# Kernel optimization log

Measured on AMD Instinct MI355X. Metric: run time of the kernel, lower is better.

## Reference

```python
import jax, jax.numpy as jnp
import numpy as np

N_HEAD = 12

def setup_inputs() -> dict:
    key = jax.random.key(0)
    ks = jax.random.split(key, 5)
    B, T, C = 2, 2048, 768
    s = 1.0 / np.sqrt(C)
    return {
        "x": jax.random.normal(ks[0], (B, T, C), dtype=jnp.float32),
        "W_qkv": jax.random.normal(ks[1], (C, 3 * C), dtype=jnp.float32) * s,
        "b_qkv": jnp.zeros((3 * C,), dtype=jnp.float32),
        "W_proj": jax.random.normal(ks[2], (C, C), dtype=jnp.float32) * s,
        "b_proj": jnp.zeros((C,), dtype=jnp.float32),
    }

def reference(x, W_qkv, b_qkv, W_proj, b_proj):
    B, T, C = x.shape
    H = N_HEAD
    D = C // H
    qkv = x @ W_qkv + b_qkv                      # [B,T,3C]
    qkv = qkv.reshape(B, T, 3, H, D)
    q = jnp.transpose(qkv[:, :, 0], (0, 2, 1, 3))  # [B,H,T,D]
    k = jnp.transpose(qkv[:, :, 1], (0, 2, 1, 3))
    v = jnp.transpose(qkv[:, :, 2], (0, 2, 1, 3))
    scale = 1.0 / np.sqrt(D).astype(np.float32)
    att = jnp.einsum('bhqd,bhkd->bhqk', q, k) * scale  # [B,H,T,T]
    causal = jnp.tril(jnp.ones((T, T), dtype=bool))
    att = jnp.where(causal, att, -jnp.inf)
    att = jax.nn.softmax(att, axis=-1)
    out = jnp.einsum('bhqk,bhkd->bhqd', att, v)   # [B,H,T,D]
    out = jnp.transpose(out, (0, 2, 1, 3)).reshape(B, T, C)
    return out @ W_proj + b_proj
```

## Files before the change

kernel.cpp:

```cpp
#include <hip/hip_runtime.h>
#include <stdint.h>

typedef short short8 __attribute__((ext_vector_type(8)));
typedef short short4v __attribute__((ext_vector_type(4)));
typedef float f32x4 __attribute__((ext_vector_type(4)));
typedef unsigned int u32x2 __attribute__((ext_vector_type(2)));
typedef unsigned int u32x4 __attribute__((ext_vector_type(4)));
typedef unsigned short u16;
typedef unsigned int u32;

#define T_ 2048
#define QK_SCALE 0.180336878f

__device__ inline u16 f2bf(float f) {
  unsigned u = __builtin_bit_cast(unsigned, f);
  u += 0x7fffu + ((u >> 16) & 1u);
  return (u16)(u >> 16);
}

__device__ inline u32 cvt_pk_bf16(float lo, float hi) {
  u32 r;
  asm("v_cvt_pk_bf16_f32 %0, %1, %2" : "=v"(r) : "v"(lo), "v"(hi));
  return r;
}

__device__ inline f32x4 mfma_bf16(short8 a, short8 b, f32x4 c) {
  return __builtin_amdgcn_mfma_f32_16x16x32_bf16(a, b, c, 0, 0, 0);
}

__device__ inline void gload16(const u16* g, u16* l) {
  __builtin_amdgcn_global_load_lds(
      (const __attribute__((address_space(1))) void*)g,
      (__attribute__((address_space(3))) void*)l, 16, 0, 0);
}


__device__ inline void tile_transpose(const float* __restrict__ W, u16* __restrict__ Wt,
                                      int R, int Ccols, int c0, int r0, int t,
                                      float (*tile)[33]) {
  int tr = t >> 3, tc = (t & 7) * 4;
  float4 v = *(const float4*)&W[(size_t)(r0 + tr) * Ccols + c0 + tc];
  tile[tr][tc + 0] = v.x; tile[tr][tc + 1] = v.y;
  tile[tr][tc + 2] = v.z; tile[tr][tc + 3] = v.w;
  __syncthreads();
  short4v o;
#pragma unroll
  for (int i = 0; i < 4; ++i) o[i] = (short)f2bf(tile[tc + i][tr]);
  *(short4v*)&Wt[(size_t)(c0 + tr) * R + r0 + tc] = o;
}

__global__ __launch_bounds__(256) void prep_kernel(const float* __restrict__ x,
                                                   const float* __restrict__ Wqkv,
                                                   const float* __restrict__ Wproj,
                                                   u16* __restrict__ xb,
                                                   u16* __restrict__ wqkvT,
                                                   u16* __restrict__ wprojT) {
  __shared__ float tile[32][33];
  int bid = blockIdx.x, t = threadIdx.x;
  if (bid < 3072) {
    int i = (bid * 256 + t) * 4;
    float4 v = *(const float4*)&x[i];
    short4v o;
    o[0] = (short)f2bf(v.x); o[1] = (short)f2bf(v.y);
    o[2] = (short)f2bf(v.z); o[3] = (short)f2bf(v.w);
    *(short4v*)&xb[i] = o;
  } else if (bid < 3072 + 1728) {
    int t2 = bid - 3072;
    tile_transpose(Wqkv, wqkvT, 768, 2304, (t2 % 72) * 32, (t2 / 72) * 32, t, tile);
  } else {
    int t3 = bid - 4800;
    tile_transpose(Wproj, wprojT, 768, 768, (t3 % 24) * 32, (t3 / 24) * 32, t, tile);
  }
}


template <int MODE, int MTILE>
__global__ __launch_bounds__(256) void gemm_kernel(const u16* __restrict__ A,
                                                   const u16* __restrict__ Bt,
                                                   const float* __restrict__ bias,
                                                   u16* __restrict__ qb,
                                                   u16* __restrict__ kb,
                                                   u16* __restrict__ vpb,
                                                   float* __restrict__ out) {
  constexpr int MF = MTILE / 32;
  __shared__ u16 S[MTILE * 64 + 8192];
  u16* As = S;
  u16* Bs = S + MTILE * 64;
  int tid = threadIdx.x, w = tid >> 6, l = tid & 63, lg = l >> 4, lr = l & 15;
  int nwg = gridDim.x * gridDim.y;
  int hw = blockIdx.y * gridDim.x + blockIdx.x;
  int logical = (hw & 7) * (nwg >> 3) + (hw >> 3);
  int n0 = (logical % gridDim.x) * 128, m0 = (logical / gridDim.x) * MTILE;
  int wm = (w >> 1) * (MTILE / 2), wn = (w & 1) * 64;
  f32x4 acc[MF][4] = {};
  int rsub = l >> 3;
  int sc = ((l & 7) ^ rsub) * 8;
  for (int kt = 0; kt < 12; ++kt) {
    int k0 = kt * 64;
    __syncthreads();
#pragma unroll
    for (int j = 0; j < MF; ++j) {
      int row = w * (MTILE / 4) + j * 8 + rsub;
      gload16(&A[(size_t)(m0 + row) * 768 + k0 + sc], &As[(w * MF + j) * 512]);
    }
#pragma unroll
    for (int j = 0; j < 4; ++j) {
      int row = w * 32 + j * 8 + rsub;
      gload16(&Bt[(size_t)(n0 + row) * 768 + k0 + sc], &Bs[(w * 4 + j) * 512]);
    }
    __syncthreads();
    short8 a[MF][2], b[4][2];
#pragma unroll
    for (int h = 0; h < 2; ++h) {
#pragma unroll
      for (int mf = 0; mf < MF; ++mf) {
        int cw = ((h * 4 + lg) ^ (lr & 7)) * 8;
        a[mf][h] = *(const short8*)&As[(wm + mf * 16 + lr) * 64 + cw];
      }
#pragma unroll
      for (int nf = 0; nf < 4; ++nf) {
        int cw = ((h * 4 + lg) ^ (lr & 7)) * 8;
        b[nf][h] = *(const short8*)&Bs[(wn + nf * 16 + lr) * 64 + cw];
      }
    }
#pragma unroll
    for (int h = 0; h < 2; ++h)
#pragma unroll
      for (int mf = 0; mf < MF; ++mf)
#pragma unroll
        for (int nf = 0; nf < 4; ++nf)
          acc[mf][nf] = mfma_bf16(a[mf][h], b[nf][h], acc[mf][nf]);
  }

  if constexpr (MODE == 0) {
    int sec = (n0 >= 1536) ? 2 : (n0 >= 768 ? 1 : 0);
    int ncol0 = n0 - sec * 768;
    if (sec < 2) {
#pragma unroll
      for (int nf = 0; nf < 4; ++nf) {
        int nn = wn + nf * 16 + lr;
        float bv = bias[n0 + nn];
        int c = ncol0 + nn;
        int hh = c >> 6, d = c & 63;
#pragma unroll
        for (int mf = 0; mf < MF; ++mf)
#pragma unroll
          for (int rr = 0; rr < 4; ++rr) {
            int m = m0 + wm + mf * 16 + 4 * lg + rr;
            int bb = m >> 11, tt = m & 2047;
            int bh = bb * 12 + hh;
            float v = acc[mf][nf][rr] + bv;
            if (sec == 0) qb[((size_t)bh * T_ + tt) * 64 + d] = f2bf(v * QK_SCALE);
            else          kb[((size_t)bh * T_ + tt) * 64 + d] = f2bf(v);
          }
      }
    } else {
      __syncthreads();
#pragma unroll
      for (int nf = 0; nf < 4; ++nf) {
        int row = wn + nf * 16 + lr;
        float bv = bias[n0 + row];
        int swz = (row & 7) << 3;
#pragma unroll
        for (int mf = 0; mf < MF; ++mf) {
          int pcol0 = wm + (mf >> 1) * 32 + 8 * lg + 4 * (mf & 1);
          u32x2 pk;
          pk[0] = cvt_pk_bf16(acc[mf][nf][0] + bv, acc[mf][nf][1] + bv);
          pk[1] = cvt_pk_bf16(acc[mf][nf][2] + bv, acc[mf][nf][3] + bv);
          *(u32x2*)&S[row * MTILE + (pcol0 ^ swz)] = pk;
        }
      }
      __syncthreads();
      constexpr int CPT = MTILE / 2;
      int rowo = tid >> 1, half = tid & 1;
      int c = ncol0 + rowo;
      int d = c & 63, hh = c >> 6;
      int bh = (m0 >> 11) * 12 + hh;
      u16* dst = vpb + ((size_t)bh * 64 + d) * T_ + (m0 & 2047) + half * CPT;
      int swzo = (rowo & 7) << 3;
#pragma unroll
      for (int i = 0; i < CPT / 8; ++i) {
        int col = half * CPT + i * 8;
        uint4 v = *(const uint4*)&S[rowo * MTILE + (col ^ swzo)];
        *(uint4*)&dst[i * 8] = v;
      }
    }
  } else {
#pragma unroll
    for (int nf = 0; nf < 4; ++nf) {
      int n = n0 + wn + nf * 16 + lr;
      float bv = bias[n];
#pragma unroll
      for (int mf = 0; mf < MF; ++mf)
#pragma unroll
        for (int rr = 0; rr < 4; ++rr) {
          int m = m0 + wm + mf * 16 + 4 * lg + rr;
          out[(size_t)m * 768 + n] = acc[mf][nf][rr] + bv;
        }
    }
  }
}


__global__ __launch_bounds__(256) void attn_kernel(const u16* __restrict__ Q,
                                                   const u16* __restrict__ K,
                                                   const u16* __restrict__ Vp,
                                                   u16* __restrict__ O) {
  __shared__ u16 sh[16384];
  int tid = threadIdx.x;
  int w = tid >> 6, l = tid & 63, lg = l >> 4, lr = l & 15;
  int idx = blockIdx.x;
  int head = idx % 24;
  int qblk = 31 - idx / 24;
  int b = head / 12, h = head % 12;
  int q0 = qblk * 64;
  int q0w = q0 + w * 16;
  const u16* Qb = Q + (size_t)head * T_ * 64;
  const u16* Kb = K + (size_t)head * T_ * 64;
  const u16* Vb = Vp + (size_t)head * 64 * T_;

  short8 qf0 = *(const short8*)&Qb[(size_t)(q0w + lr) * 64 + 8 * lg];
  short8 qf1 = *(const short8*)&Qb[(size_t)(q0w + lr) * 64 + 32 + 8 * lg];

  f32x4 ao[4] = {};
  float lrow = 0.f;
  int rsub = l >> 3;
  int scs = ((l & 7) ^ rsub) * 8;
  const int nt = qblk + 1;

#pragma unroll
  for (int j = 0; j < 2; ++j) {
    int ci = w * 2 + j;
    int row = ci * 8 + rsub;
    gload16(&Kb[(size_t)row * 64 + scs], &sh[ci * 512]);
    gload16(&Vb[(size_t)row * T_ + scs], &sh[8192 + ci * 512]);
  }
  __syncthreads();

  for (int t = 0; t < nt; ++t) {
    int cur = t & 1;
    int k0 = t * 64;
    if (t + 1 < nt) {
      int k1 = k0 + 64;
#pragma unroll
      for (int j = 0; j < 2; ++j) {
        int ci = w * 2 + j;
        int row = ci * 8 + rsub;
        gload16(&Kb[(size_t)(k1 + row) * 64 + scs], &sh[(cur ^ 1) * 4096 + ci * 512]);
        gload16(&Vb[(size_t)row * T_ + k1 + scs], &sh[8192 + (cur ^ 1) * 4096 + ci * 512]);
      }
    }
    if (k0 <= q0w + 15) {
      const u16* ks = sh + cur * 4096;
      const u16* vs = sh + 8192 + cur * 4096;
      f32x4 s[4];
      __builtin_amdgcn_s_setprio(1);
#pragma unroll
      for (int kg = 0; kg < 4; ++kg) {
        short8 ka0 = *(const short8*)&ks[(kg * 16 + lr) * 64 + ((lg ^ (lr & 7)) * 8)];
        short8 ka1 = *(const short8*)&ks[(kg * 16 + lr) * 64 + (((4 + lg) ^ (lr & 7)) * 8)];
        f32x4 z = {};
        z = mfma_bf16(ka0, qf0, z);
        z = mfma_bf16(ka1, qf1, z);
        s[kg] = z;
      }
      __builtin_amdgcn_s_setprio(0);
      int qa = q0w + lr;
      bool domask = (k0 + 63 > q0w);
      float sv[16];
      float ps = 0.f;
#pragma unroll
      for (int kg = 0; kg < 4; ++kg)
#pragma unroll
        for (int rr = 0; rr < 4; ++rr) {
          float x = s[kg][rr];
          if (domask) {
            int key = k0 + kg * 16 + 4 * lg + rr;
            x = (key <= qa) ? x : -1e30f;
          }
          float p = __builtin_amdgcn_exp2f(x);
          sv[kg * 4 + rr] = p;
          ps += p;
        }
      ps += __shfl_xor(ps, 16);
      ps += __shfl_xor(ps, 32);
      lrow += ps;
      short8 pb[2];
#pragma unroll
      for (int c = 0; c < 2; ++c) {
        u32x4 uu;
        uu[0] = cvt_pk_bf16(sv[c * 8 + 0], sv[c * 8 + 1]);
        uu[1] = cvt_pk_bf16(sv[c * 8 + 2], sv[c * 8 + 3]);
        uu[2] = cvt_pk_bf16(sv[c * 8 + 4], sv[c * 8 + 5]);
        uu[3] = cvt_pk_bf16(sv[c * 8 + 6], sv[c * 8 + 7]);
        pb[c] = __builtin_bit_cast(short8, uu);
      }
      __builtin_amdgcn_s_setprio(1);
#pragma unroll
      for (int dt = 0; dt < 4; ++dt) {
        short8 va0 = *(const short8*)&vs[(dt * 16 + lr) * 64 + ((lg ^ (lr & 7)) * 8)];
        short8 va1 = *(const short8*)&vs[(dt * 16 + lr) * 64 + (((4 + lg) ^ (lr & 7)) * 8)];
        ao[dt] = mfma_bf16(va0, pb[0], ao[dt]);
        ao[dt] = mfma_bf16(va1, pb[1], ao[dt]);
      }
      __builtin_amdgcn_s_setprio(0);
    }
    __syncthreads();
  }

  u16* ow = sh + w * 1152;
  float inv = 1.0f / lrow;
#pragma unroll
  for (int dt = 0; dt < 4; ++dt) {
    u32x2 pk;
    pk[0] = cvt_pk_bf16(ao[dt][0] * inv, ao[dt][1] * inv);
    pk[1] = cvt_pk_bf16(ao[dt][2] * inv, ao[dt][3] * inv);
    *(u32x2*)&ow[lr * 72 + dt * 16 + 4 * lg] = pk;
  }
  __syncthreads();
  int r = l >> 2, hc = l & 3;
  const u16* srow = sh + w * 1152 + r * 72 + hc * 16;
  u16* dst = O + ((size_t)(b * T_ + q0w + r)) * 768 + h * 64 + hc * 16;
  *(uint4*)&dst[0] = *(const uint4*)&srow[0];
  *(uint4*)&dst[8] = *(const uint4*)&srow[8];
}


extern "C" void kernel_launch(void* const* d_in, const int* in_sizes, int n_in,
                              void* d_out, int out_size, void* d_ws, size_t ws_size,
                              hipStream_t stream) {
  const float* x     = (const float*)d_in[0];
  const float* Wqkv  = (const float*)d_in[1];
  const float* bqkv  = (const float*)d_in[2];
  const float* Wproj = (const float*)d_in[3];
  const float* bproj = (const float*)d_in[4];
  float* out = (float*)d_out;
  char* ws = (char*)d_ws;
  u16* xb     = (u16*)(ws);
  u16* wqkvT  = (u16*)(ws + 6291456);
  u16* wprojT = (u16*)(ws + 9830400);
  u16* qb     = (u16*)(ws + 11010048);
  u16* kb     = (u16*)(ws + 17301504);
  u16* vpb    = (u16*)(ws + 23592960);
  u16* ob     = (u16*)(ws + 29884416);

  prep_kernel<<<5376, 256, 0, stream>>>(x, Wqkv, Wproj, xb, wqkvT, wprojT);
  gemm_kernel<0, 64><<<dim3(18, 64), 256, 0, stream>>>(xb, wqkvT, bqkv, qb, kb, vpb, nullptr);
  attn_kernel<<<768, 256, 0, stream>>>(qb, kb, vpb, ob);
  gemm_kernel<1, 64><<<dim3(6, 64), 256, 0, stream>>>(ob, wprojT, bproj, nullptr, nullptr, nullptr, out);
}
```

Measured before the change: 86.27 us.

## Split long causal attention query blocks across two workgroups with a combine pass

Query blocks 16–31, which carry the longest causal key ranges, are now split in half along the key dimension. Each half is computed by its own workgroup and writes unnormalised bf16 partial outputs and row sums into reused workspace buffers. A new combine kernel adds the two halves and normalises them. The aim is to balance load and raise the number of workgroups in flight. The cost is an extra kernel launch, more global traffic, and an extra bf16 rounding of the partial sums.

```diff
diff --git a/kernel.cpp b/kernel.cpp
--- a/kernel.cpp
+++ b/kernel.cpp
@@ -16,6 +16,10 @@
   unsigned u = __builtin_bit_cast(unsigned, f);
   u += 0x7fffu + ((u >> 16) & 1u);
   return (u16)(u >> 16);
+}
+
+__device__ inline float bf2f(u16 v) {
+  return __builtin_bit_cast(float, (u32)v << 16);
 }
 
 __device__ inline u32 cvt_pk_bf16(float lo, float hi) {
@@ -205,15 +209,21 @@
 __global__ __launch_bounds__(256) void attn_kernel(const u16* __restrict__ Q,
                                                    const u16* __restrict__ K,
                                                    const u16* __restrict__ Vp,
-                                                   u16* __restrict__ O) {
+                                                   u16* __restrict__ O,
+                                                   u16* __restrict__ Pp,
+                                                   float* __restrict__ Lp) {
   __shared__ u16 sh[16384];
   int tid = threadIdx.x;
   int w = tid >> 6, l = tid & 63, lg = l >> 4, lr = l & 15;
-  int idx = blockIdx.x;
-  int head = idx % 24;
-  int qblk = 31 - idx / 24;
+  int u = blockIdx.x;
+  int head = u % 24;
+  int v = u / 24;
+  int s, c;
+  if (v < 32) { s = 31 - (v >> 1); c = v & 1; }
+  else        { s = 47 - v; c = 0; }
+  bool ispartial = (v < 32);
   int b = head / 12, h = head % 12;
-  int q0 = qblk * 64;
+  int q0 = s * 64;
   int q0w = q0 + w * 16;
   const u16* Qb = Q + (size_t)head * T_ * 64;
   const u16* Kb = K + (size_t)head * T_ * 64;
@@ -226,21 +236,24 @@
   float lrow = 0.f;
   int rsub = l >> 3;
   int scs = ((l & 7) ^ rsub) * 8;
-  const int nt = qblk + 1;
+  int nt = s + 1;
+  int h1 = (s + 2) >> 1;
+  int t0 = (ispartial && c) ? h1 : 0;
+  int tEnd = (ispartial && !c) ? h1 : nt;
 
 #pragma unroll
   for (int j = 0; j < 2; ++j) {
     int ci = w * 2 + j;
     int row = ci * 8 + rsub;
-    gload16(&Kb[(size_t)row * 64 + scs], &sh[ci * 512]);
-    gload16(&Vb[(size_t)row * T_ + scs], &sh[8192 + ci * 512]);
+    gload16(&Kb[(size_t)(t0 * 64 + row) * 64 + scs], &sh[ci * 512]);
+    gload16(&Vb[(size_t)row * T_ + t0 * 64 + scs], &sh[8192 + ci * 512]);
   }
   __syncthreads();
 
-  for (int t = 0; t < nt; ++t) {
-    int cur = t & 1;
+  for (int t = t0; t < tEnd; ++t) {
+    int cur = (t - t0) & 1;
     int k0 = t * 64;
-    if (t + 1 < nt) {
+    if (t + 1 < tEnd) {
       int k1 = k0 + 64;
 #pragma unroll
       for (int j = 0; j < 2; ++j) {
@@ -253,7 +266,7 @@
     if (k0 <= q0w + 15) {
       const u16* ks = sh + cur * 4096;
       const u16* vs = sh + 8192 + cur * 4096;
-      f32x4 s[4];
+      f32x4 sm[4];
       __builtin_amdgcn_s_setprio(1);
 #pragma unroll
       for (int kg = 0; kg < 4; ++kg) {
@@ -262,7 +275,7 @@
         f32x4 z = {};
         z = mfma_bf16(ka0, qf0, z);
         z = mfma_bf16(ka1, qf1, z);
-        s[kg] = z;
+        sm[kg] = z;
       }
       __builtin_amdgcn_s_setprio(0);
       int qa = q0w + lr;
@@ -273,7 +286,7 @@
       for (int kg = 0; kg < 4; ++kg)
 #pragma unroll
         for (int rr = 0; rr < 4; ++rr) {
-          float x = s[kg][rr];
+          float x = sm[kg][rr];
           if (domask) {
             int key = k0 + kg * 16 + 4 * lg + rr;
             x = (key <= qa) ? x : -1e30f;
@@ -287,13 +300,13 @@
       lrow += ps;
       short8 pb[2];
 #pragma unroll
-      for (int c = 0; c < 2; ++c) {
+      for (int c2 = 0; c2 < 2; ++c2) {
         u32x4 uu;
-        uu[0] = cvt_pk_bf16(sv[c * 8 + 0], sv[c * 8 + 1]);
-        uu[1] = cvt_pk_bf16(sv[c * 8 + 2], sv[c * 8 + 3]);
-        uu[2] = cvt_pk_bf16(sv[c * 8 + 4], sv[c * 8 + 5]);
-        uu[3] = cvt_pk_bf16(sv[c * 8 + 6], sv[c * 8 + 7]);
-        pb[c] = __builtin_bit_cast(short8, uu);
+        uu[0] = cvt_pk_bf16(sv[c2 * 8 + 0], sv[c2 * 8 + 1]);
+        uu[1] = cvt_pk_bf16(sv[c2 * 8 + 2], sv[c2 * 8 + 3]);
+        uu[2] = cvt_pk_bf16(sv[c2 * 8 + 4], sv[c2 * 8 + 5]);
+        uu[3] = cvt_pk_bf16(sv[c2 * 8 + 6], sv[c2 * 8 + 7]);
+        pb[c2] = __builtin_bit_cast(short8, uu);
       }
       __builtin_amdgcn_s_setprio(1);
 #pragma unroll
@@ -309,7 +322,7 @@
   }
 
   u16* ow = sh + w * 1152;
-  float inv = 1.0f / lrow;
+  float inv = ispartial ? 1.0f : (1.0f / lrow);
 #pragma unroll
   for (int dt = 0; dt < 4; ++dt) {
     u32x2 pk;
@@ -320,9 +333,38 @@
   __syncthreads();
   int r = l >> 2, hc = l & 3;
   const u16* srow = sh + w * 1152 + r * 72 + hc * 16;
-  u16* dst = O + ((size_t)(b * T_ + q0w + r)) * 768 + h * 64 + hc * 16;
-  *(uint4*)&dst[0] = *(const uint4*)&srow[0];
-  *(uint4*)&dst[8] = *(const uint4*)&srow[8];
+  if (!ispartial) {
+    u16* dst = O + ((size_t)(b * T_ + q0w + r)) * 768 + h * 64 + hc * 16;
+    *(uint4*)&dst[0] = *(const uint4*)&srow[0];
+    *(uint4*)&dst[8] = *(const uint4*)&srow[8];
+  } else {
+    int pidx = (head * 16 + (s - 16)) * 2 + c;
+    u16* dst = Pp + (size_t)pidx * 4096 + (w * 16 + r) * 64 + hc * 16;
+    *(uint4*)&dst[0] = *(const uint4*)&srow[0];
+    *(uint4*)&dst[8] = *(const uint4*)&srow[8];
+    if (lg == 0) Lp[pidx * 64 + w * 16 + lr] = lrow;
+  }
+}
+
+__global__ __launch_bounds__(256) void combine_kernel(const u16* __restrict__ Pp,
+                                                      const float* __restrict__ Lp,
+                                                      u16* __restrict__ O) {
+  int d = threadIdx.x & 63;
+  int u = blockIdx.x * 4 + (threadIdx.x >> 6);
+  int head = u % 24;
+  int s = 16 + u / 24;
+  int b = head / 12, h = head % 12;
+  int p0 = (head * 16 + (s - 16)) * 2;
+  const u16* P0 = Pp + (size_t)p0 * 4096;
+  const u16* P1 = P0 + 4096;
+  const float* L0 = Lp + p0 * 64;
+  const float* L1 = L0 + 64;
+#pragma unroll 4
+  for (int q = 0; q < 64; ++q) {
+    float o = bf2f(P0[q * 64 + d]) + bf2f(P1[q * 64 + d]);
+    float ls = L0[q] + L1[q];
+    O[((size_t)(b * T_ + s * 64 + q)) * 768 + h * 64 + d] = f2bf(o / ls);
+  }
 }
 
 
@@ -343,9 +385,12 @@
   u16* kb     = (u16*)(ws + 17301504);
   u16* vpb    = (u16*)(ws + 23592960);
   u16* ob     = (u16*)(ws + 29884416);
+  u16* Pp = xb;
+  float* Lp = (float*)wqkvT;
 
   prep_kernel<<<5376, 256, 0, stream>>>(x, Wqkv, Wproj, xb, wqkvT, wprojT);
   gemm_kernel<0, 64><<<dim3(18, 64), 256, 0, stream>>>(xb, wqkvT, bqkv, qb, kb, vpb, nullptr);
-  attn_kernel<<<768, 256, 0, stream>>>(qb, kb, vpb, ob);
+  attn_kernel<<<1152, 256, 0, stream>>>(qb, kb, vpb, ob, Pp, Lp);
+  combine_kernel<<<96, 256, 0, stream>>>(Pp, Lp, ob);
   gemm_kernel<1, 64><<<dim3(6, 64), 256, 0, stream>>>(ob, wprojT, bproj, nullptr, nullptr, nullptr, out);
 }
```

Result: slower. 94.72 us (+9.8%).
